# Optimization experiments

Hardware: AMD Instinct MI355X
Metric: run time of the kernel (lower is better)

The kernel has to match this reference:

```python
import jax, jax.numpy as jnp
import numpy as np

T_STEPS = 256   # euler ODE steps
B = 1024        # batch (trajectories)
D = 64          # input_size
H = 768         # hidden_size
PH = 512        # p_hidden
P = 10          # prep_hidden
COV = 32        # cov_size
COVH = 128      # cov_hidden
DELTA_T = 0.05
MIXING = 1.0
VAR_EPS = 1e-6


def _xavier(k, out_f, in_f):
    lim = float(np.sqrt(6.0 / (in_f + out_f)))
    return jax.random.uniform(k, (out_f, in_f), minval=-lim, maxval=lim, dtype=jnp.float32)


def setup_inputs():
    key = jax.random.key(0)
    ks = jax.random.split(key, 16)
    return {
        "X": jax.random.normal(ks[0], (T_STEPS, B, D), jnp.float32),
        "M": jnp.ones((T_STEPS, B, D), jnp.float32),
        "obs_mask": jax.random.randint(ks[1], (T_STEPS, B), 0, 2).astype(bool),
        "cov": jax.random.normal(ks[2], (B, COV), jnp.float32),
        # GRU-ODE cell (input is p, size 2*D)
        "Wxz": _xavier(ks[3], H, 2 * D), "bxz": jnp.full((H,), 0.05, jnp.float32),
        "Wxn": _xavier(ks[4], H, 2 * D), "bxn": jnp.full((H,), 0.05, jnp.float32),
        "Whz": _xavier(ks[5], H, H), "Whn": _xavier(ks[6], H, H),
        # p_model
        "Wp1": _xavier(ks[7], PH, H), "bp1": jnp.full((PH,), 0.05, jnp.float32),
        "Wp2": _xavier(ks[8], 2 * D, PH), "bp2": jnp.full((2 * D,), 0.05, jnp.float32),
        # covariates_map
        "Wc1": _xavier(ks[9], COVH, COV), "bc1": jnp.full((COVH,), 0.05, jnp.float32),
        "Wc2": _xavier(ks[10], H, COVH), "bc2": jnp.full((H,), 0.05, jnp.float32),
        # observation GRUCell (torch.nn.GRUCell layout: r,z,n chunks)
        "Wih": _xavier(ks[11], 3 * H, P * D), "Whh": _xavier(ks[12], 3 * H, H),
        "bih": jnp.zeros((3 * H,), jnp.float32), "bhh": jnp.zeros((3 * H,), jnp.float32),
        "w_prep": float(np.sqrt(2.0 / (4 + P))) * jax.random.normal(ks[13], (D, 4, P), jnp.float32),
        "bias_prep": jnp.full((D, P), 0.1, jnp.float32),
    }


def reference(X, M, obs_mask, cov, Wxz, bxz, Wxn, bxn, Whz, Whn,
              Wp1, bp1, Wp2, bp2, Wc1, bc1, Wc2, bc2,
              Wih, Whh, bih, bhh, w_prep, bias_prep):
    p_model = lambda h: jax.nn.relu(h @ Wp1.T + bp1) @ Wp2.T + bp2

    def gru_ode(p, h):  # minimal GRU-ODE cell, returns dh/dt
        z = jax.nn.sigmoid(p @ Wxz.T + bxz + h @ Whz.T)
        n = jnp.tanh(p @ Wxn.T + bxn + (z * h) @ Whn.T)
        return (1.0 - z) * (n - h)

    def gru_cell(x, h):  # torch.nn.GRUCell
        gi = x @ Wih.T + bih
        gh = h @ Whh.T + bhh
        ir, iz, inn = jnp.split(gi, 3, axis=1)
        hr, hz, hn = jnp.split(gh, 3, axis=1)
        r = jax.nn.sigmoid(ir + hr)
        z = jax.nn.sigmoid(iz + hz)
        n = jnp.tanh(inn + r * hn)
        return (1.0 - z) * n + z * h

    def nll(p, Xt, Mm):  # gaussian NLL with |var|+eps (use_logvar=False path)
        mean, var = jnp.split(p, 2, axis=1)
        av = jnp.abs(var) + VAR_EPS
        err = (Xt - mean) / jnp.sqrt(av)
        return 0.5 * ((err * err + jnp.log(av)) * Mm).sum(), mean, av, err

    def step(carry, inp):
        h, loss = carry
        Xt, Mt, om = inp
        p = p_model(h)
        h = h + DELTA_T * gru_ode(p, h)          # euler ODE step (impute=True feeds p)
        p = p_model(h)
        Mm = Mt * om[:, None].astype(Mt.dtype)   # actually-observed entries this step
        loss_pre, mean, av, err = nll(p, Xt, Mm)
        gi = jnp.stack([Xt, mean, av, err], axis=2)                         # [B, D, 4]
        gi = jax.nn.relu(jnp.einsum('bdf,dfp->bdp', gi, w_prep) + bias_prep)
        gi = (gi * Mm[:, :, None]).reshape(Xt.shape[0], -1)                 # [B, D*P]
        h_new = gru_cell(gi, h)
        h = jnp.where(om[:, None], h_new, h)      # Bayesian jump only on observed rows
        loss_post, _, _, _ = nll(p_model(h), Xt, Mm)
        return (h, loss + loss_pre + MIXING * loss_post), None

    h0 = jnp.tanh(jax.nn.relu(cov @ Wc1.T + bc1) @ Wc2.T + bc2)
    (h, loss), _ = jax.lax.scan(step, (h0, jnp.float32(0.0)), (X, M, obs_mask))
    return h, loss
```

## Files before the change

### kernel.cpp

```cpp
#include <hip/hip_runtime.h>

typedef unsigned short u16;
typedef __attribute__((ext_vector_type(4))) float f32x4;
typedef __attribute__((ext_vector_type(8))) short short8;

#define NUM_T 256
#define BATCH 1024
#define DIM 64
#define HID 768
#define PHID 512
#define PREP 10
#define GIN 640
#define COVSZ 32
#define COVH 128
#define DT_ 0.05f
#define VEPS 1e-6f
#define NTH 512
#define NWAVE 8
#define NWG 256
#define GQ 4
#define GROUPS 64

#define LHB 776
#define LPH 520
#define LPF 132
#define LPB 136
#define LZH 776
#define LGI 648

struct Params {
  const float *X, *M; const int *obs; const float *cov;
  const float *bxz, *bxn, *bp1, *bp2, *bc1, *bc2, *bih, *bhh, *wprep, *bprep;
  const float *Wc1, *Wc2;
  const u16 *Wxz, *Wxn, *Whz, *Whn, *Wp1, *Wp2, *Wih, *Whh;
  float *out_h; float *partials; u16 *exch; unsigned *cnt;
};

__device__ __forceinline__ u16 f2bf(float f){
  unsigned u = __builtin_bit_cast(unsigned, f);
  u = (u + 0x7FFFu + ((u >> 16) & 1u)) >> 16;
  return (u16)u;
}
__device__ __forceinline__ float bf2f(u16 h){
  unsigned u = ((unsigned)h) << 16;
  return __builtin_bit_cast(float, u);
}
__device__ __forceinline__ float sigm(float x){ return 1.0f/(1.0f + __expf(-x)); }
__device__ __forceinline__ float tanh_f(float x){
  float t = __expf(-2.0f*fabsf(x));
  float r = (1.0f - t)/(1.0f + t);
  return x >= 0.0f ? r : -r;
}

struct Smem {
  u16   h_b[16*LHB];
  u16   z_b[16*LHB];
  float p_f[16*LPF];
  u16   p_b[16*LPB];
  union {
    u16 zh[16*LZH];
    u16 gi[16*LGI];
    u16 ph1[16*LPH];
  } u;
  int om[2][16];
  float red[NWAVE];
};

template<int NKC, int NT>
__device__ __forceinline__ void dotP(const u16* __restrict__ A, int lda,
    const u16* __restrict__ W2, int tile0, f32x4* acc,
    int c, int g, int lane, int w)
{
  static_assert((NKC & 1) == 0, "NKC must be even");
  const u16* a = A + c*lda + g*8;
  const short8* base[NT];
  #pragma unroll
  for (int j = 0; j < NT; ++j)
    base[j] = (const short8*)(W2 + ((size_t)(tile0 + w + 8*j)*NKC)*512) + lane;
  short8 ldA[NT], ldB[NT];
  #pragma unroll
  for (int j = 0; j < NT; ++j) ldA[j] = base[j][0];
  #pragma unroll
  for (int j = 0; j < NT; ++j) ldB[j] = base[j][64];
  __builtin_amdgcn_s_barrier();
  #pragma unroll 1
  for (int kp = 0; kp < NKC/2 - 1; ++kp){
    int kk = 2*kp;
    {
      short8 av = *(const short8*)(a + 32*kk);
      #pragma unroll
      for (int j = 0; j < NT; ++j)
        acc[j] = __builtin_amdgcn_mfma_f32_16x16x32_bf16(av, ldA[j], acc[j], 0, 0, 0);
      #pragma unroll
      for (int j = 0; j < NT; ++j) ldA[j] = base[j][64*(kk + 2)];
      __builtin_amdgcn_s_barrier();
    }
    {
      short8 av = *(const short8*)(a + 32*(kk + 1));
      #pragma unroll
      for (int j = 0; j < NT; ++j)
        acc[j] = __builtin_amdgcn_mfma_f32_16x16x32_bf16(av, ldB[j], acc[j], 0, 0, 0);
      #pragma unroll
      for (int j = 0; j < NT; ++j) ldB[j] = base[j][64*(kk + 3)];
      __builtin_amdgcn_s_barrier();
    }
  }
  {
    short8 av = *(const short8*)(a + 32*(NKC - 2));
    #pragma unroll
    for (int j = 0; j < NT; ++j)
      acc[j] = __builtin_amdgcn_mfma_f32_16x16x32_bf16(av, ldA[j], acc[j], 0, 0, 0);
    __builtin_amdgcn_s_barrier();
    av = *(const short8*)(a + 32*(NKC - 1));
    #pragma unroll
    for (int j = 0; j < NT; ++j)
      acc[j] = __builtin_amdgcn_mfma_f32_16x16x32_bf16(av, ldB[j], acc[j], 0, 0, 0);
    __builtin_amdgcn_s_barrier();
  }
}

template<int NKC>
__device__ __forceinline__ void dotPG(const u16* __restrict__ A, int lda,
    const u16* __restrict__ W2, int t0, int t1, bool v1, f32x4* acc,
    int c, int g, int lane)
{
  static_assert((NKC & 1) == 0, "NKC must be even");
  const u16* a = A + c*lda + g*8;
  const short8* b0 = (const short8*)(W2 + ((size_t)t0*NKC)*512) + lane;
  const short8* b1 = (const short8*)(W2 + ((size_t)t1*NKC)*512) + lane;
  short8 A0, A1v, B0, B1v;
  A0 = b0[0]; B0 = b0[64];
  if (v1){ A1v = b1[0]; B1v = b1[64]; }
  __builtin_amdgcn_s_barrier();
  #pragma unroll 1
  for (int kp = 0; kp < NKC/2 - 1; ++kp){
    int kk = 2*kp;
    {
      short8 av = *(const short8*)(a + 32*kk);
      acc[0] = __builtin_amdgcn_mfma_f32_16x16x32_bf16(av, A0, acc[0], 0, 0, 0);
      if (v1) acc[1] = __builtin_amdgcn_mfma_f32_16x16x32_bf16(av, A1v, acc[1], 0, 0, 0);
      A0 = b0[64*(kk + 2)];
      if (v1) A1v = b1[64*(kk + 2)];
      __builtin_amdgcn_s_barrier();
    }
    {
      short8 av = *(const short8*)(a + 32*(kk + 1));
      acc[0] = __builtin_amdgcn_mfma_f32_16x16x32_bf16(av, B0, acc[0], 0, 0, 0);
      if (v1) acc[1] = __builtin_amdgcn_mfma_f32_16x16x32_bf16(av, B1v, acc[1], 0, 0, 0);
      B0 = b0[64*(kk + 3)];
      if (v1) B1v = b1[64*(kk + 3)];
      __builtin_amdgcn_s_barrier();
    }
  }
  {
    short8 av = *(const short8*)(a + 32*(NKC - 2));
    acc[0] = __builtin_amdgcn_mfma_f32_16x16x32_bf16(av, A0, acc[0], 0, 0, 0);
    if (v1) acc[1] = __builtin_amdgcn_mfma_f32_16x16x32_bf16(av, A1v, acc[1], 0, 0, 0);
    __builtin_amdgcn_s_barrier();
    av = *(const short8*)(a + 32*(NKC - 1));
    acc[0] = __builtin_amdgcn_mfma_f32_16x16x32_bf16(av, B0, acc[0], 0, 0, 0);
    if (v1) acc[1] = __builtin_amdgcn_mfma_f32_16x16x32_bf16(av, B1v, acc[1], 0, 0, 0);
    __builtin_amdgcn_s_barrier();
  }
}

template<int NKC>
__device__ __forceinline__ void dot3PG(const u16* __restrict__ A, int lda,
    const u16* __restrict__ W2, int t0, bool act, f32x4* acc, int c, int g, int lane)
{
  static_assert((NKC & 1) == 0, "NKC must be even");
  const u16* a = A + c*lda + g*8;
  const short8* base[3];
  #pragma unroll
  for (int j = 0; j < 3; ++j)
    base[j] = (const short8*)(W2 + ((size_t)(t0 + 48*j)*NKC)*512) + lane;
  short8 ldA[3], ldB[3];
  if (act){
    #pragma unroll
    for (int j = 0; j < 3; ++j) ldA[j] = base[j][0];
    #pragma unroll
    for (int j = 0; j < 3; ++j) ldB[j] = base[j][64];
  }
  __builtin_amdgcn_s_barrier();
  #pragma unroll 1
  for (int kp = 0; kp < NKC/2 - 1; ++kp){
    int kk = 2*kp;
    if (act){
      short8 av = *(const short8*)(a + 32*kk);
      #pragma unroll
      for (int j = 0; j < 3; ++j)
        acc[j] = __builtin_amdgcn_mfma_f32_16x16x32_bf16(av, ldA[j], acc[j], 0, 0, 0);
      #pragma unroll
      for (int j = 0; j < 3; ++j) ldA[j] = base[j][64*(kk + 2)];
      av = *(const short8*)(a + 32*(kk + 1));
      #pragma unroll
      for (int j = 0; j < 3; ++j)
        acc[j] = __builtin_amdgcn_mfma_f32_16x16x32_bf16(av, ldB[j], acc[j], 0, 0, 0);
      #pragma unroll
      for (int j = 0; j < 3; ++j) ldB[j] = base[j][64*(kk + 3)];
    }
    __builtin_amdgcn_s_barrier();
  }
  if (act){
    short8 av = *(const short8*)(a + 32*(NKC - 2));
    #pragma unroll
    for (int j = 0; j < 3; ++j)
      acc[j] = __builtin_amdgcn_mfma_f32_16x16x32_bf16(av, ldA[j], acc[j], 0, 0, 0);
    av = *(const short8*)(a + 32*(NKC - 1));
    #pragma unroll
    for (int j = 0; j < 3; ++j)
      acc[j] = __builtin_amdgcn_mfma_f32_16x16x32_bf16(av, ldB[j], acc[j], 0, 0, 0);
  }
  __builtin_amdgcn_s_barrier();
}

__device__ __forceinline__ void dotPB16(const u16* __restrict__ A, int lda,
    const u16* __restrict__ W2, f32x4* acc, int c, int g, int lane, int w)
{
  const u16* a = A + c*lda + g*8;
  const short8* base = (const short8*)(W2 + ((size_t)w*16)*512) + lane;
  short8 ldA[4], ldB[4];
  #pragma unroll
  for (int m = 0; m < 4; ++m) ldA[m] = base[64*m];
  #pragma unroll
  for (int m = 0; m < 4; ++m) ldB[m] = base[64*(4 + m)];
  __builtin_amdgcn_s_barrier();
  #pragma unroll
  for (int m = 0; m < 4; ++m){
    short8 av = *(const short8*)(a + 32*m);
    acc[0] = __builtin_amdgcn_mfma_f32_16x16x32_bf16(av, ldA[m], acc[0], 0, 0, 0);
  }
  #pragma unroll
  for (int m = 0; m < 4; ++m) ldA[m] = base[64*(8 + m)];
  __builtin_amdgcn_s_barrier();
  #pragma unroll
  for (int m = 0; m < 4; ++m){
    short8 av = *(const short8*)(a + 32*(4 + m));
    acc[0] = __builtin_amdgcn_mfma_f32_16x16x32_bf16(av, ldB[m], acc[0], 0, 0, 0);
  }
  #pragma unroll
  for (int m = 0; m < 4; ++m) ldB[m] = base[64*(12 + m)];
  __builtin_amdgcn_s_barrier();
  #pragma unroll
  for (int m = 0; m < 4; ++m){
    short8 av = *(const short8*)(a + 32*(8 + m));
    acc[0] = __builtin_amdgcn_mfma_f32_16x16x32_bf16(av, ldA[m], acc[0], 0, 0, 0);
  }
  __builtin_amdgcn_s_barrier();
  #pragma unroll
  for (int m = 0; m < 4; ++m){
    short8 av = *(const short8*)(a + 32*(12 + m));
    acc[0] = __builtin_amdgcn_mfma_f32_16x16x32_bf16(av, ldB[m], acc[0], 0, 0, 0);
  }
  __builtin_amdgcn_s_barrier();
}

__global__ __launch_bounds__(NTH)
void nnfo_main(Params pr)
{
  __shared__ Smem sm;
  const int tid  = threadIdx.x;
  const int lane = tid & 63;
  const int w    = tid >> 6;
  const int c = lane & 15;
  const int g = lane >> 4;
  const int b = blockIdx.x;
  const int q    = (b >> 3) & 3;
  const int G    = (b & 7)*8 + (b >> 5);
  const int row0 = G * 16;

  u16* exZH = pr.exch + (size_t)G*32768;
  u16* exH  = exZH + 16*HID;
  u16* exP1 = exH  + 16*HID;
  unsigned* cnt = pr.cnt + G*16;

  unsigned gen = 0;
  auto gsync = [&](){
    __syncthreads();
    if (tid == 0)
      __hip_atomic_fetch_add(cnt, 1u, __ATOMIC_RELEASE, __HIP_MEMORY_SCOPE_AGENT);
    gen += GQ;
    if (tid == 0){
      int spins = 0;
      while (__hip_atomic_load(cnt, __ATOMIC_ACQUIRE, __HIP_MEMORY_SCOPE_AGENT) < gen){
        __builtin_amdgcn_s_sleep(1);
        if (++spins > 8000000) break;
      }
    }
    __syncthreads();
  };
  auto copyLDS = [&](u16* dst, int ldst, const u16* src, int wcols){
    int nb = 16*(wcols >> 3);
    for (int idx = tid; idx < nb; idx += NTH){
      int r = idx/(wcols >> 3), cb = idx - r*(wcols >> 3);
      *(short8*)(dst + r*ldst + cb*8) = *(const short8*)(src + (size_t)r*wcols + cb*8);
    }
    __syncthreads();
  };

  const int  tA0 = q*12 + w;
  const int  tA1 = (w < 4) ? (q*12 + w + 8) : (q*12 + w);
  const bool vA1 = (w < 4);
  const int  tP  = q*8 + w;

  float loss = 0.0f;
  float hreg[2][4];

  for (int it = tid; it < 16*COVH; it += NTH){
    int r = it >> 7, j = it & 127;
    float acc = pr.bc1[j];
    const float* cv = pr.cov + (size_t)(row0 + r)*COVSZ;
    const float* wv = pr.Wc1 + (size_t)j*COVSZ;
    for (int k = 0; k < COVSZ; ++k) acc += cv[k]*wv[k];
    sm.p_f[r*LPF + j] = fmaxf(acc, 0.0f);
  }
  __syncthreads();
  for (int it = tid; it < 16*HID; it += NTH){
    int r = it / HID, j = it - r*HID;
    float acc = pr.bc2[j];
    const float* wv = pr.Wc2 + (size_t)j*COVH;
    for (int k = 0; k < COVH; ++k) acc += sm.p_f[r*LPF + k]*wv[k];
    sm.h_b[r*LHB + j] = f2bf(tanh_f(acc));
  }
  #pragma unroll
  for (int s = 0; s < 2; ++s){
    bool act = (s == 0) || vA1;
    int tt = s ? tA1 : tA0;
    int n = tt*16 + c;
    const float* wv = pr.Wc2 + (size_t)n*COVH;
    #pragma unroll
    for (int i = 0; i < 4; ++i){
      int r = g*4 + i;
      float acc = pr.bc2[n];
      for (int k = 0; k < COVH; ++k) acc += sm.p_f[r*LPF + k]*wv[k];
      hreg[s][i] = act ? tanh_f(acc) : 0.0f;
    }
  }
  __syncthreads();

  auto pm1G = [&](){
    f32x4 acc[1] = {};
    dotP<24, 1>(sm.h_b, LHB, pr.Wp1, q*8, acc, c, g, lane, w);
    int n = tP*16 + c;
    float bb = pr.bp1[n];
    #pragma unroll
    for (int i = 0; i < 4; ++i)
      exP1[(size_t)(g*4 + i)*PHID + n] = f2bf(fmaxf(acc[0][i] + bb, 0.0f));
    gsync();
    copyLDS(sm.u.ph1, LPH, exP1, PHID);
  };
  auto pm2R = [&](bool write_pb){
    f32x4 acc[1] = {};
    dotPB16(sm.u.ph1, LPH, pr.Wp2, acc, c, g, lane, w);
    int n = w*16 + c;
    float bb = pr.bp2[n];
    #pragma unroll
    for (int i = 0; i < 4; ++i){
      float v = acc[0][i] + bb;
      sm.p_f[(g*4 + i)*LPF + n] = v;
      if (write_pb) sm.p_b[(g*4 + i)*LPB + n] = f2bf(v);
    }
    __syncthreads();
  };

  pm1G();
  pm2R(true);

  float Xs[2], Ms[2];

  #pragma unroll 1
  for (int t = 0; t < NUM_T; ++t){
    if (tid < 16) sm.om[t & 1][tid] = pr.obs[(size_t)t*BATCH + row0 + tid];
    float Xpre[2];
    #pragma unroll
    for (int q2 = 0; q2 < 2; ++q2){
      int it = tid + q2*NTH;
      int r = it >> 6, d = it & 63;
      Xpre[q2] = pr.X[((size_t)t*BATCH + row0 + r)*DIM + d];
    }

    {
      f32x4 accz[2] = {};
      dotPG<4>(sm.p_b, LPB, pr.Wxz, tA0, tA1, vA1, accz, c, g, lane);
      dotPG<24>(sm.h_b, LHB, pr.Whz, tA0, tA1, vA1, accz, c, g, lane);
      #pragma unroll
      for (int s = 0; s < 2; ++s){
        bool act = (s == 0) || vA1;
        if (act){
          int tt = s ? tA1 : tA0;
          int n = tt*16 + c;
          float bb = pr.bxz[n];
          #pragma unroll
          for (int i = 0; i < 4; ++i){
            int r = g*4 + i;
            float z = sigm(accz[s][i] + bb);
            sm.z_b[r*LHB + n] = f2bf(z);
            exZH[(size_t)r*HID + n] = f2bf(z*hreg[s][i]);
          }
        }
      }
      gsync();
      copyLDS(sm.u.zh, LZH, exZH, HID);
    }
    {
      f32x4 accn[2] = {};
      dotPG<4>(sm.p_b, LPB, pr.Wxn, tA0, tA1, vA1, accn, c, g, lane);
      dotPG<24>(sm.u.zh, LZH, pr.Whn, tA0, tA1, vA1, accn, c, g, lane);
      #pragma unroll
      for (int s = 0; s < 2; ++s){
        bool act = (s == 0) || vA1;
        if (act){
          int tt = s ? tA1 : tA0;
          int n = tt*16 + c;
          float bb = pr.bxn[n];
          #pragma unroll
          for (int i = 0; i < 4; ++i){
            int r = g*4 + i;
            float nv = tanh_f(accn[s][i] + bb);
            float z  = bf2f(sm.z_b[r*LHB + n]);
            float h  = hreg[s][i];
            h = h + DT_*(1.0f - z)*(nv - h);
            hreg[s][i] = h;
            exH[(size_t)r*HID + n] = f2bf(h);
          }
        }
      }
      gsync();
      copyLDS(sm.h_b, LHB, exH, HID);
    }

    pm1G();
    pm2R(false);

    #pragma unroll
    for (int q2 = 0; q2 < 2; ++q2){
      int it = tid + q2*NTH;
      int r = it >> 6, d = it & 63;
      size_t xoff = ((size_t)t*BATCH + row0 + r)*DIM + d;
      float Xv = Xpre[q2];
      float om = sm.om[t & 1][r] ? 1.0f : 0.0f;
      float Mv = pr.M[xoff] * om;
      Xs[q2] = Xv; Ms[q2] = Mv;
      float mean = sm.p_f[r*LPF + d];
      float var  = sm.p_f[r*LPF + 64 + d];
      float av   = fabsf(var) + VEPS;
      float inv  = rsqrtf(av);
      float errv = (Xv - mean)*inv;
      if (q == 0) loss += 0.5f*(errv*errv + __logf(av))*Mv;
      #pragma unroll
      for (int p = 0; p < PREP; ++p){
        float s = pr.bprep[d*PREP + p]
                + Xv  * pr.wprep[(d*4 + 0)*PREP + p]
                + mean* pr.wprep[(d*4 + 1)*PREP + p]
                + av  * pr.wprep[(d*4 + 2)*PREP + p]
                + errv* pr.wprep[(d*4 + 3)*PREP + p];
        sm.u.gi[r*LGI + d*PREP + p] = f2bf(fmaxf(s, 0.0f)*Mv);
      }
    }
    __syncthreads();

    {
      float hn_buf[2][4];
      #pragma unroll 1
      for (int s = 0; s < 2; ++s){
        bool act = (s == 0) || vA1;
        int ht = s ? tA1 : tA0;
        int n = ht*16 + c;
        f32x4 ai[3] = {};
        dot3PG<20>(sm.u.gi, LGI, pr.Wih, ht, act, ai, c, g, lane);
        f32x4 ah[3] = {};
        dot3PG<24>(sm.h_b, LHB, pr.Whh, ht, act, ah, c, g, lane);
        #pragma unroll
        for (int i = 0; i < 4; ++i){
          float ir = ai[0][i] + pr.bih[n];
          float iz = ai[1][i] + pr.bih[HID + n];
          float in = ai[2][i] + pr.bih[2*HID + n];
          float hr = ah[0][i] + pr.bhh[n];
          float hz = ah[1][i] + pr.bhh[HID + n];
          float hn = ah[2][i] + pr.bhh[2*HID + n];
          float rr  = sigm(ir + hr);
          float zz  = sigm(iz + hz);
          float nn  = tanh_f(in + rr*hn);
          hn_buf[s][i] = (1.0f - zz)*nn + zz*hreg[s][i];
        }
      }
      #pragma unroll
      for (int s = 0; s < 2; ++s){
        bool act = (s == 0) || vA1;
        if (act){
          int tt = s ? tA1 : tA0;
          int n = tt*16 + c;
          #pragma unroll
          for (int i = 0; i < 4; ++i){
            int r = g*4 + i;
            if (sm.om[t & 1][r]) hreg[s][i] = hn_buf[s][i];
            exH[(size_t)r*HID + n] = f2bf(hreg[s][i]);
          }
        }
      }
      gsync();
      copyLDS(sm.h_b, LHB, exH, HID);
    }

    pm1G();
    pm2R(true);

    if (q == 0){
      #pragma unroll
      for (int q2 = 0; q2 < 2; ++q2){
        int it = tid + q2*NTH;
        int r = it >> 6, d = it & 63;
        float mean = sm.p_f[r*LPF + d];
        float var  = sm.p_f[r*LPF + 64 + d];
        float av   = fabsf(var) + VEPS;
        float inv  = rsqrtf(av);
        float errv = (Xs[q2] - mean)*inv;
        loss += 0.5f*(errv*errv + __logf(av))*Ms[q2];
      }
    }
  }

  __syncthreads();
  #pragma unroll
  for (int s = 0; s < 2; ++s){
    bool act = (s == 0) || vA1;
    if (act){
      int tt = s ? tA1 : tA0;
      int n = tt*16 + c;
      #pragma unroll
      for (int i = 0; i < 4; ++i){
        int r = g*4 + i;
        pr.out_h[(size_t)(row0 + r)*HID + n] = hreg[s][i];
      }
    }
  }
  #pragma unroll
  for (int off = 32; off >= 1; off >>= 1) loss += __shfl_down(loss, off);
  if (lane == 0) sm.red[w] = loss;
  __syncthreads();
  if (tid == 0 && q == 0){
    float ssum = 0.0f;
    for (int i = 0; i < NWAVE; ++i) ssum += sm.red[i];
    pr.partials[G] = ssum;
  }
}

__global__ void k_swz(const float* __restrict__ s, u16* __restrict__ d, int N, int K){
  int i = blockIdx.x*blockDim.x + threadIdx.x;
  if (i >= N*K) return;
  int e    = i & 7;
  int lane = (i >> 3) & 63;
  int rest = i >> 9;
  int ks = K >> 5;
  int k = rest % ks, t = rest / ks;
  int cc = lane & 15, gg = lane >> 4;
  d[i] = f2bf(s[(size_t)(t*16 + cc)*K + (k*32 + gg*8 + e)]);
}

__global__ void k_final(const float* __restrict__ partials, float* __restrict__ out_loss){
  float v = (threadIdx.x < GROUPS) ? partials[threadIdx.x] : 0.0f;
  #pragma unroll
  for (int off = 32; off >= 1; off >>= 1) v += __shfl_down(v, off);
  if (threadIdx.x == 0) out_loss[0] = v;
}

extern "C" void kernel_launch(void* const* d_in, const int* in_sizes, int n_in,
                              void* d_out, int out_size, void* d_ws, size_t ws_size,
                              hipStream_t stream)
{
  const float* X   = (const float*)d_in[0];
  const float* M   = (const float*)d_in[1];
  const int*   obs = (const int*)  d_in[2];
  const float* cov = (const float*)d_in[3];
  const float* Wxz = (const float*)d_in[4];
  const float* bxz = (const float*)d_in[5];
  const float* Wxn = (const float*)d_in[6];
  const float* bxn = (const float*)d_in[7];
  const float* Whz = (const float*)d_in[8];
  const float* Whn = (const float*)d_in[9];
  const float* Wp1 = (const float*)d_in[10];
  const float* bp1 = (const float*)d_in[11];
  const float* Wp2 = (const float*)d_in[12];
  const float* bp2 = (const float*)d_in[13];
  const float* Wc1 = (const float*)d_in[14];
  const float* bc1 = (const float*)d_in[15];
  const float* Wc2 = (const float*)d_in[16];
  const float* bc2 = (const float*)d_in[17];
  const float* Wih = (const float*)d_in[18];
  const float* Whh = (const float*)d_in[19];
  const float* bih = (const float*)d_in[20];
  const float* bhh = (const float*)d_in[21];
  const float* wprep = (const float*)d_in[22];
  const float* bprep = (const float*)d_in[23];

  u16* w = (u16*)d_ws;
  u16* wXZ = w + 0;
  u16* wXN = w + 98304;
  u16* wHZ = w + 196608;
  u16* wHN = w + 786432;
  u16* wP1 = w + 1376256;
  u16* wP2 = w + 1769472;
  u16* wIH = w + 1835008;
  u16* wHH = w + 3309568;
  float*    partials = (float*)((char*)d_ws + 10158080);
  unsigned* cnt      = (unsigned*)((char*)d_ws + 10158336);
  u16*      exch     = (u16*)((char*)d_ws + 10162432);

  struct CV { const float* s; u16* d; int N; int K; } cvs[8] = {
    {Wxz, wXZ, 768, 128}, {Wxn, wXN, 768, 128}, {Whz, wHZ, 768, 768}, {Whn, wHN, 768, 768},
    {Wp1, wP1, 512, 768}, {Wp2, wP2, 128, 512}, {Wih, wIH, 2304, 640}, {Whh, wHH, 2304, 768},
  };
  for (int i = 0; i < 8; ++i){
    int n = cvs[i].N * cvs[i].K;
    k_swz<<<(n + 255)/256, 256, 0, stream>>>(cvs[i].s, cvs[i].d, cvs[i].N, cvs[i].K);
  }
  hipMemsetAsync(cnt, 0, 4096, stream);

  Params pr { X, M, obs, cov, bxz, bxn, bp1, bp2, bc1, bc2, bih, bhh, wprep, bprep,
              Wc1, Wc2, wXZ, wXN, wHZ, wHN, wP1, wP2, wIH, wHH,
              (float*)d_out, partials, exch, cnt };
  nnfo_main<<<NWG, NTH, 0, stream>>>(pr);
  k_final<<<1, 64, 0, stream>>>(partials, (float*)d_out + (size_t)BATCH*HID);
}
```

Baseline: 26.27 ms.

## Deepen weight prefetch to four stages and overlap Wxn GEMV with group barrier

The dot-product helpers now keep four register-resident weight fragments in flight instead of two, with the loop restructured around steps of four K-chunks and guarded prefetches. The group barrier is split into a signal half and a wait half, so the p·Wxn partial product runs while waiting for the other workgroups' z·h exchange. The aim is to hide global weight-load latency and barrier spin time, at the cost of more VGPRs, which could lower occupancy or cause spills.

```diff
diff --git a/kernel.cpp b/kernel.cpp
--- a/kernel.cpp
+++ b/kernel.cpp
@@ -28,6 +28,8 @@
 #define LZH 776
 #define LGI 648
 
+#define MFMA_ __builtin_amdgcn_mfma_f32_16x16x32_bf16
+
 struct Params {
   const float *X, *M; const int *obs; const float *cov;
   const float *bxz, *bxn, *bp1, *bp2, *bc1, *bc2, *bih, *bhh, *wprep, *bprep;
@@ -71,51 +73,65 @@
     const u16* __restrict__ W2, int tile0, f32x4* acc,
     int c, int g, int lane, int w)
 {
-  static_assert((NKC & 1) == 0, "NKC must be even");
+  static_assert((NKC & 3) == 0, "NKC % 4");
   const u16* a = A + c*lda + g*8;
   const short8* base[NT];
   #pragma unroll
   for (int j = 0; j < NT; ++j)
     base[j] = (const short8*)(W2 + ((size_t)(tile0 + w + 8*j)*NKC)*512) + lane;
-  short8 ldA[NT], ldB[NT];
-  #pragma unroll
-  for (int j = 0; j < NT; ++j) ldA[j] = base[j][0];
-  #pragma unroll
-  for (int j = 0; j < NT; ++j) ldB[j] = base[j][64];
+  short8 sA[NT], sB[NT], sC[NT], sD[NT];
+  #pragma unroll
+  for (int j = 0; j < NT; ++j) sA[j] = base[j][0];
+  #pragma unroll
+  for (int j = 0; j < NT; ++j) sB[j] = base[j][64];
+  #pragma unroll
+  for (int j = 0; j < NT; ++j) sC[j] = base[j][128];
+  #pragma unroll
+  for (int j = 0; j < NT; ++j) sD[j] = base[j][192];
   __builtin_amdgcn_s_barrier();
   #pragma unroll 1
-  for (int kp = 0; kp < NKC/2 - 1; ++kp){
-    int kk = 2*kp;
+  for (int kp = 0; kp < NKC/4; ++kp){
+    int kk = 4*kp;
     {
       short8 av = *(const short8*)(a + 32*kk);
       #pragma unroll
-      for (int j = 0; j < NT; ++j)
-        acc[j] = __builtin_amdgcn_mfma_f32_16x16x32_bf16(av, ldA[j], acc[j], 0, 0, 0);
-      #pragma unroll
-      for (int j = 0; j < NT; ++j) ldA[j] = base[j][64*(kk + 2)];
+      for (int j = 0; j < NT; ++j) acc[j] = MFMA_(av, sA[j], acc[j], 0, 0, 0);
+      if (kk + 4 < NKC){
+        #pragma unroll
+        for (int j = 0; j < NT; ++j) sA[j] = base[j][64*(kk + 4)];
+      }
       __builtin_amdgcn_s_barrier();
     }
     {
       short8 av = *(const short8*)(a + 32*(kk + 1));
       #pragma unroll
-      for (int j = 0; j < NT; ++j)
-        acc[j] = __builtin_amdgcn_mfma_f32_16x16x32_bf16(av, ldB[j], acc[j], 0, 0, 0);
-      #pragma unroll
-      for (int j = 0; j < NT; ++j) ldB[j] = base[j][64*(kk + 3)];
-      __builtin_amdgcn_s_barrier();
-    }
-  }
-  {
-    short8 av = *(const short8*)(a + 32*(NKC - 2));
-    #pragma unroll
-    for (int j = 0; j < NT; ++j)
-      acc[j] = __builtin_amdgcn_mfma_f32_16x16x32_bf16(av, ldA[j], acc[j], 0, 0, 0);
-    __builtin_amdgcn_s_barrier();
-    av = *(const short8*)(a + 32*(NKC - 1));
-    #pragma unroll
-    for (int j = 0; j < NT; ++j)
-      acc[j] = __builtin_amdgcn_mfma_f32_16x16x32_bf16(av, ldB[j], acc[j], 0, 0, 0);
-    __builtin_amdgcn_s_barrier();
+      for (int j = 0; j < NT; ++j) acc[j] = MFMA_(av, sB[j], acc[j], 0, 0, 0);
+      if (kk + 5 < NKC){
+        #pragma unroll
+        for (int j = 0; j < NT; ++j) sB[j] = base[j][64*(kk + 5)];
+      }
+      __builtin_amdgcn_s_barrier();
+    }
+    {
+      short8 av = *(const short8*)(a + 32*(kk + 2));
+      #pragma unroll
+      for (int j = 0; j < NT; ++j) acc[j] = MFMA_(av, sC[j], acc[j], 0, 0, 0);
+      if (kk + 6 < NKC){
+        #pragma unroll
+        for (int j = 0; j < NT; ++j) sC[j] = base[j][64*(kk + 6)];
+      }
+      __builtin_amdgcn_s_barrier();
+    }
+    {
+      short8 av = *(const short8*)(a + 32*(kk + 3));
+      #pragma unroll
+      for (int j = 0; j < NT; ++j) acc[j] = MFMA_(av, sD[j], acc[j], 0, 0, 0);
+      if (kk + 7 < NKC){
+        #pragma unroll
+        for (int j = 0; j < NT; ++j) sD[j] = base[j][64*(kk + 7)];
+      }
+      __builtin_amdgcn_s_barrier();
+    }
   }
 }
 
@@ -124,43 +140,45 @@
     const u16* __restrict__ W2, int t0, int t1, bool v1, f32x4* acc,
     int c, int g, int lane)
 {
-  static_assert((NKC & 1) == 0, "NKC must be even");
+  static_assert((NKC & 3) == 0, "NKC % 4");
   const u16* a = A + c*lda + g*8;
   const short8* b0 = (const short8*)(W2 + ((size_t)t0*NKC)*512) + lane;
   const short8* b1 = (const short8*)(W2 + ((size_t)t1*NKC)*512) + lane;
-  short8 A0, A1v, B0, B1v;
-  A0 = b0[0]; B0 = b0[64];
-  if (v1){ A1v = b1[0]; B1v = b1[64]; }
+  short8 A0, B0, C0, D0, A1, B1, C1, D1;
+  A0 = b0[0]; B0 = b0[64]; C0 = b0[128]; D0 = b0[192];
+  if (v1){ A1 = b1[0]; B1 = b1[64]; C1 = b1[128]; D1 = b1[192]; }
   __builtin_amdgcn_s_barrier();
   #pragma unroll 1
-  for (int kp = 0; kp < NKC/2 - 1; ++kp){
-    int kk = 2*kp;
+  for (int kp = 0; kp < NKC/4; ++kp){
+    int kk = 4*kp;
     {
       short8 av = *(const short8*)(a + 32*kk);
-      acc[0] = __builtin_amdgcn_mfma_f32_16x16x32_bf16(av, A0, acc[0], 0, 0, 0);
-      if (v1) acc[1] = __builtin_amdgcn_mfma_f32_16x16x32_bf16(av, A1v, acc[1], 0, 0, 0);
-      A0 = b0[64*(kk + 2)];
-      if (v1) A1v = b1[64*(kk + 2)];
+      acc[0] = MFMA_(av, A0, acc[0], 0, 0, 0);
+      if (v1) acc[1] = MFMA_(av, A1, acc[1], 0, 0, 0);
+      if (kk + 4 < NKC){ A0 = b0[64*(kk + 4)]; if (v1) A1 = b1[64*(kk + 4)]; }
       __builtin_amdgcn_s_barrier();
     }
     {
       short8 av = *(const short8*)(a + 32*(kk + 1));
-      acc[0] = __builtin_amdgcn_mfma_f32_16x16x32_bf16(av, B0, acc[0], 0, 0, 0);
-      if (v1) acc[1] = __builtin_amdgcn_mfma_f32_16x16x32_bf16(av, B1v, acc[1], 0, 0, 0);
-      B0 = b0[64*(kk + 3)];
-      if (v1) B1v = b1[64*(kk + 3)];
-      __builtin_amdgcn_s_barrier();
-    }
-  }
-  {
-    short8 av = *(const short8*)(a + 32*(NKC - 2));
-    acc[0] = __builtin_amdgcn_mfma_f32_16x16x32_bf16(av, A0, acc[0], 0, 0, 0);
-    if (v1) acc[1] = __builtin_amdgcn_mfma_f32_16x16x32_bf16(av, A1v, acc[1], 0, 0, 0);
-    __builtin_amdgcn_s_barrier();
-    av = *(const short8*)(a + 32*(NKC - 1));
-    acc[0] = __builtin_amdgcn_mfma_f32_16x16x32_bf16(av, B0, acc[0], 0, 0, 0);
-    if (v1) acc[1] = __builtin_amdgcn_mfma_f32_16x16x32_bf16(av, B1v, acc[1], 0, 0, 0);
-    __builtin_amdgcn_s_barrier();
+      acc[0] = MFMA_(av, B0, acc[0], 0, 0, 0);
+      if (v1) acc[1] = MFMA_(av, B1, acc[1], 0, 0, 0);
+      if (kk + 5 < NKC){ B0 = b0[64*(kk + 5)]; if (v1) B1 = b1[64*(kk + 5)]; }
+      __builtin_amdgcn_s_barrier();
+    }
+    {
+      short8 av = *(const short8*)(a + 32*(kk + 2));
+      acc[0] = MFMA_(av, C0, acc[0], 0, 0, 0);
+      if (v1) acc[1] = MFMA_(av, C1, acc[1], 0, 0, 0);
+      if (kk + 6 < NKC){ C0 = b0[64*(kk + 6)]; if (v1) C1 = b1[64*(kk + 6)]; }
+      __builtin_amdgcn_s_barrier();
+    }
+    {
+      short8 av = *(const short8*)(a + 32*(kk + 3));
+      acc[0] = MFMA_(av, D0, acc[0], 0, 0, 0);
+      if (v1) acc[1] = MFMA_(av, D1, acc[1], 0, 0, 0);
+      if (kk + 7 < NKC){ D0 = b0[64*(kk + 7)]; if (v1) D1 = b1[64*(kk + 7)]; }
+      __builtin_amdgcn_s_barrier();
+    }
   }
 }
 
@@ -168,50 +186,68 @@
 __device__ __forceinline__ void dot3PG(const u16* __restrict__ A, int lda,
     const u16* __restrict__ W2, int t0, bool act, f32x4* acc, int c, int g, int lane)
 {
-  static_assert((NKC & 1) == 0, "NKC must be even");
+  static_assert((NKC & 3) == 0, "NKC % 4");
   const u16* a = A + c*lda + g*8;
   const short8* base[3];
   #pragma unroll
   for (int j = 0; j < 3; ++j)
     base[j] = (const short8*)(W2 + ((size_t)(t0 + 48*j)*NKC)*512) + lane;
-  short8 ldA[3], ldB[3];
+  short8 sA[3], sB[3], sC[3], sD[3];
   if (act){
     #pragma unroll
-    for (int j = 0; j < 3; ++j) ldA[j] = base[j][0];
-    #pragma unroll
-    for (int j = 0; j < 3; ++j) ldB[j] = base[j][64];
+    for (int j = 0; j < 3; ++j) sA[j] = base[j][0];
+    #pragma unroll
+    for (int j = 0; j < 3; ++j) sB[j] = base[j][64];
+    #pragma unroll
+    for (int j = 0; j < 3; ++j) sC[j] = base[j][128];
+    #pragma unroll
+    for (int j = 0; j < 3; ++j) sD[j] = base[j][192];
   }
   __builtin_amdgcn_s_barrier();
   #pragma unroll 1
-  for (int kp = 0; kp < NKC/2 - 1; ++kp){
-    int kk = 2*kp;
+  for (int kp = 0; kp < NKC/4; ++kp){
+    int kk = 4*kp;
     if (act){
       short8 av = *(const short8*)(a + 32*kk);
       #pragma unroll
-      for (int j = 0; j < 3; ++j)
-        acc[j] = __builtin_amdgcn_mfma_f32_16x16x32_bf16(av, ldA[j], acc[j], 0, 0, 0);
-      #pragma unroll
-      for (int j = 0; j < 3; ++j) ldA[j] = base[j][64*(kk + 2)];
-      av = *(const short8*)(a + 32*(kk + 1));
-      #pragma unroll
-      for (int j = 0; j < 3; ++j)
-        acc[j] = __builtin_amdgcn_mfma_f32_16x16x32_bf16(av, ldB[j], acc[j], 0, 0, 0);
-      #pragma unroll
-      for (int j = 0; j < 3; ++j) ldB[j] = base[j][64*(kk + 3)];
+      for (int j = 0; j < 3; ++j) acc[j] = MFMA_(av, sA[j], acc[j], 0, 0, 0);
+      if (kk + 4 < NKC){
+        #pragma unroll
+        for (int j = 0; j < 3; ++j) sA[j] = base[j][64*(kk + 4)];
+      }
     }
     __builtin_amdgcn_s_barrier();
-  }
-  if (act){
-    short8 av = *(const short8*)(a + 32*(NKC - 2));
-    #pragma unroll
-    for (int j = 0; j < 3; ++j)
-      acc[j] = __builtin_amdgcn_mfma_f32_16x16x32_bf16(av, ldA[j], acc[j], 0, 0, 0);
-    av = *(const short8*)(a + 32*(NKC - 1));
-    #pragma unroll
-    for (int j = 0; j < 3; ++j)
-      acc[j] = __builtin_amdgcn_mfma_f32_16x16x32_bf16(av, ldB[j], acc[j], 0, 0, 0);
-  }
-  __builtin_amdgcn_s_barrier();
+    if (act){
+      short8 av = *(const short8*)(a + 32*(kk + 1));
+      #pragma unroll
+      for (int j = 0; j < 3; ++j) acc[j] = MFMA_(av, sB[j], acc[j], 0, 0, 0);
+      if (kk + 5 < NKC){
+        #pragma unroll
+        for (int j = 0; j < 3; ++j) sB[j] = base[j][64*(kk + 5)];
+      }
+    }
+    __builtin_amdgcn_s_barrier();
+    if (act){
+      short8 av = *(const short8*)(a + 32*(kk + 2));
+      #pragma unroll
+      for (int j = 0; j < 3; ++j) acc[j] = MFMA_(av, sC[j], acc[j], 0, 0, 0);
+      if (kk + 6 < NKC){
+        #pragma unroll
+        for (int j = 0; j < 3; ++j) sC[j] = base[j][64*(kk + 6)];
+      }
+    }
+    __builtin_amdgcn_s_barrier();
+    if (act){
+      short8 av = *(const short8*)(a + 32*(kk + 3));
+      #pragma unroll
+      for (int j = 0; j < 3; ++j) acc[j] = MFMA_(av, sD[j], acc[j], 0, 0, 0);
+      if (kk + 7 < NKC){
+        #pragma unroll
+        for (int j = 0; j < 3; ++j) sD[j] = base[j][64*(kk + 7)];
+      }
+    }
+    __builtin_amdgcn_s_barrier();
+  }
 }
 
 __device__ __forceinline__ void dotPB16(const u16* __restrict__ A, int lda,
@@ -228,7 +264,7 @@
   #pragma unroll
   for (int m = 0; m < 4; ++m){
     short8 av = *(const short8*)(a + 32*m);
-    acc[0] = __builtin_amdgcn_mfma_f32_16x16x32_bf16(av, ldA[m], acc[0], 0, 0, 0);
+    acc[0] = MFMA_(av, ldA[m], acc[0], 0, 0, 0);
   }
   #pragma unroll
   for (int m = 0; m < 4; ++m) ldA[m] = base[64*(8 + m)];
@@ -236,7 +272,7 @@
   #pragma unroll
   for (int m = 0; m < 4; ++m){
     short8 av = *(const short8*)(a + 32*(4 + m));
-    acc[0] = __builtin_amdgcn_mfma_f32_16x16x32_bf16(av, ldB[m], acc[0], 0, 0, 0);
+    acc[0] = MFMA_(av, ldB[m], acc[0], 0, 0, 0);
   }
   #pragma unroll
   for (int m = 0; m < 4; ++m) ldB[m] = base[64*(12 + m)];
@@ -244,13 +280,13 @@
   #pragma unroll
   for (int m = 0; m < 4; ++m){
     short8 av = *(const short8*)(a + 32*(8 + m));
-    acc[0] = __builtin_amdgcn_mfma_f32_16x16x32_bf16(av, ldA[m], acc[0], 0, 0, 0);
+    acc[0] = MFMA_(av, ldA[m], acc[0], 0, 0, 0);
   }
   __builtin_amdgcn_s_barrier();
   #pragma unroll
   for (int m = 0; m < 4; ++m){
     short8 av = *(const short8*)(a + 32*(12 + m));
-    acc[0] = __builtin_amdgcn_mfma_f32_16x16x32_bf16(av, ldB[m], acc[0], 0, 0, 0);
+    acc[0] = MFMA_(av, ldB[m], acc[0], 0, 0, 0);
   }
   __builtin_amdgcn_s_barrier();
 }
@@ -275,11 +311,13 @@
   unsigned* cnt = pr.cnt + G*16;
 
   unsigned gen = 0;
-  auto gsync = [&](){
+  auto gsig = [&](){
     __syncthreads();
     if (tid == 0)
       __hip_atomic_fetch_add(cnt, 1u, __ATOMIC_RELEASE, __HIP_MEMORY_SCOPE_AGENT);
     gen += GQ;
+  };
+  auto gwait = [&](){
     if (tid == 0){
       int spins = 0;
       while (__hip_atomic_load(cnt, __ATOMIC_ACQUIRE, __HIP_MEMORY_SCOPE_AGENT) < gen){
@@ -346,7 +384,8 @@
     #pragma unroll
     for (int i = 0; i < 4; ++i)
       exP1[(size_t)(g*4 + i)*PHID + n] = f2bf(fmaxf(acc[0][i] + bb, 0.0f));
-    gsync();
+    gsig();
+    gwait();
     copyLDS(sm.u.ph1, LPH, exP1, PHID);
   };
   auto pm2R = [&](bool write_pb){
@@ -378,6 +417,8 @@
       int r = it >> 6, d = it & 63;
       Xpre[q2] = pr.X[((size_t)t*BATCH + row0 + r)*DIM + d];
     }
+
+    f32x4 accn[2] = {};
 
     {
       f32x4 accz[2] = {};
@@ -399,12 +440,12 @@
           }
         }
       }
-      gsync();
+      gsig();
+      dotPG<4>(sm.p_b, LPB, pr.Wxn, tA0, tA1, vA1, accn, c, g, lane);
+      gwait();
       copyLDS(sm.u.zh, LZH, exZH, HID);
     }
     {
-      f32x4 accn[2] = {};
-      dotPG<4>(sm.p_b, LPB, pr.Wxn, tA0, tA1, vA1, accn, c, g, lane);
       dotPG<24>(sm.u.zh, LZH, pr.Whn, tA0, tA1, vA1, accn, c, g, lane);
       #pragma unroll
       for (int s = 0; s < 2; ++s){
@@ -425,7 +466,8 @@
           }
         }
       }
-      gsync();
+      gsig();
+      gwait();
       copyLDS(sm.h_b, LHB, exH, HID);
     }
 
@@ -498,7 +540,8 @@
           }
         }
       }
-      gsync();
+      gsig();
+      gwait();
       copyLDS(sm.h_b, LHB, exH, HID);
     }
 
```

After: 28.65 ms. +9.0%, slower.
